# Kernel tuning notes

Measured on AMD Instinct MI355X. Metric: run time of the kernel, lower is better.

## Reference

```python
import jax, jax.numpy as jnp
import numpy as np

H, C = 3, 64  # heads, per-head channels
NEG_SLOPE = 0.2

def setup_inputs() -> dict:
    key = jax.random.key(0)
    ks = jax.random.split(key, 8)
    B, N, D, E = 2, 50000, 128, 800000
    h = jax.random.normal(ks[0], (B, N, D), dtype=jnp.float32)
    edge_index = jax.random.randint(ks[1], (2, E), 0, N, dtype=jnp.int64)
    s = 1.0 / np.sqrt(D)
    W = jax.random.normal(ks[2], (D, H * C), dtype=jnp.float32) * s
    a_src = jax.random.normal(ks[3], (H, C), dtype=jnp.float32) * (1.0 / np.sqrt(C))
    a_dst = jax.random.normal(ks[4], (H, C), dtype=jnp.float32) * (1.0 / np.sqrt(C))
    bias = jnp.zeros((H * C,), dtype=jnp.float32)
    Wo = jax.random.normal(ks[5], (H * C, 1), dtype=jnp.float32) * (1.0 / np.sqrt(H * C))
    bo = jnp.zeros((1,), dtype=jnp.float32)
    return {"h": h, "edge_index": edge_index, "W": W, "a_src": a_src,
            "a_dst": a_dst, "bias": bias, "Wo": Wo, "bo": bo}

def _gat_single(h_b, src, dst, N, W, a_src, a_dst, bias):
    # h_b: [N, D] -> x: [N, H, C]
    x = (h_b @ W).reshape(-1, H, C)
    alpha_s = jnp.einsum('nhc,hc->nh', x, a_src)  # [N, H]
    alpha_d = jnp.einsum('nhc,hc->nh', x, a_dst)  # [N, H]
    e = alpha_s[src] + alpha_d[dst]               # [E', H]
    e = jnp.where(e > 0, e, NEG_SLOPE * e)        # leaky_relu(0.2)
    # segment softmax over edges grouped by destination node
    emax = jax.ops.segment_max(e, dst, num_segments=N)          # [N, H]
    p = jnp.exp(e - emax[dst])
    denom = jax.ops.segment_sum(p, dst, num_segments=N)         # [N, H]
    att = p / (denom[dst] + 1e-16)                               # [E', H]
    out = jax.ops.segment_sum(att[:, :, None] * x[src], dst, num_segments=N)  # [N,H,C]
    return out.reshape(-1, H * C) + bias

def reference(h, edge_index, W, a_src, a_dst, bias, Wo, bo):
    B, N, D = h.shape
    # PyG GATConv default: add self loops
    loops = jnp.arange(N, dtype=edge_index.dtype)
    src = jnp.concatenate([edge_index[0], loops])
    dst = jnp.concatenate([edge_index[1], loops])
    gat = jax.vmap(lambda hb: _gat_single(hb, src, dst, N, W, a_src, a_dst, bias))(h)
    gat = jax.nn.elu(gat)            # [B, N, H*C]; dropout inactive (eval)
    logits = gat @ Wo + bo           # [B, N, 1]
    return logits
```

## Files before the change

### kernel.cpp

```cpp
#include <hip/hip_runtime.h>
#include <hip/hip_bf16.h>
#include <math.h>

typedef __hip_bfloat16 bf16;
typedef __attribute__((ext_vector_type(8))) short short8;
typedef __attribute__((ext_vector_type(4))) float f32x4;

#define HC 192
#define DIN 128
#define NEG_SLOPE 0.2f
#define LCH 64

static inline int cdiv(int a, int b){ return (a + b - 1) / b; }

__device__ inline short f2bf(float f){
  __hip_bfloat16 b = __float2bfloat16(f);
  return __builtin_bit_cast(short, b);
}
__device__ inline float loadf(const void* p, size_t i, int fm){
  return fm ? __bfloat162float(((const bf16*)p)[i]) : ((const float*)p)[i];
}
__device__ inline int eload(const void* p, long long i, int em){
  return em ? (int)(((const long long*)p)[i]) : ((const int*)p)[i];
}

__device__ inline int detect_fm(const unsigned* __restrict__ hw){
  unsigned w = hw[threadIdx.x & 63];
  unsigned expo = (w >> 7) & 0xFF;
  unsigned long long m = __ballot(expo >= 100 && expo <= 135);
  return __popcll(m) > 32;
}
__device__ inline int detect_em(const unsigned* __restrict__ ew){
  unsigned long long m = __ballot(ew[2*(threadIdx.x & 63) + 1] != 0);
  return __popcll(m) < 32;
}

__global__ void k_repack(const void* __restrict__ W, const void* __restrict__ a_src,
    const void* __restrict__ a_dst, const void* __restrict__ bias,
    const void* __restrict__ Wo, const void* __restrict__ bo,
    const unsigned* __restrict__ hw, bf16* __restrict__ Wt,
    float* __restrict__ asf, float* __restrict__ adf, float* __restrict__ biasf,
    float* __restrict__ Wof, float* __restrict__ bof){
  int fm = detect_fm(hw);
  int idx = blockIdx.x * 256 + threadIdx.x;
  if (idx < DIN * HC){
    int d = idx / HC, j = idx - d * HC;
    Wt[j * DIN + d] = __float2bfloat16(loadf(W, idx, fm));
  }
  if (idx < HC){
    asf[idx]   = loadf(a_src, idx, fm);
    adf[idx]   = loadf(a_dst, idx, fm);
    biasf[idx] = loadf(bias, idx, fm);
    Wof[idx]   = loadf(Wo, idx, fm);
  }
  if (idx == 0) bof[0] = loadf(bo, 0, fm);
}

__global__ __launch_bounds__(256) void k_gemm(const void* __restrict__ h,
    const bf16* __restrict__ Wt, bf16* __restrict__ x,
    const float* __restrict__ asf, const float* __restrict__ adf,
    float* __restrict__ asp, float* __restrict__ adp, int M, int N){
  int fm   = detect_fm((const unsigned*)h);
  int tid  = threadIdx.x;
  int w    = tid >> 6;
  int lane = tid & 63;
  int r16  = lane & 15;
  int quad = lane >> 4;
  __shared__ short ldsW[HC * 136];
  for (int c = tid; c < HC * 16; c += 256){
    int row = c >> 4, kg = c & 15;
    *(short8*)&ldsW[row * 136 + kg * 8] = *(const short8*)(Wt + row * DIN + kg * 8);
  }
  __syncthreads();

  int row  = blockIdx.x * 64 + w * 16 + r16;
  int lrow = min(row, M - 1);
  f32x4 acc[12];
  #pragma unroll
  for (int i = 0; i < 12; i++) acc[i] = (f32x4){0.f,0.f,0.f,0.f};
  size_t abase = (size_t)lrow * DIN + quad * 8;
  #pragma unroll
  for (int kb = 0; kb < 4; kb++){
    short8 af;
    if (fm == 0){
      const float* hf = (const float*)h + abase + kb * 32;
      float4 a = *(const float4*)hf;
      float4 b = *(const float4*)(hf + 4);
      af[0]=f2bf(a.x); af[1]=f2bf(a.y); af[2]=f2bf(a.z); af[3]=f2bf(a.w);
      af[4]=f2bf(b.x); af[5]=f2bf(b.y); af[6]=f2bf(b.z); af[7]=f2bf(b.w);
    } else {
      af = *(const short8*)((const bf16*)h + abase + kb * 32);
    }
    #pragma unroll
    for (int nt = 0; nt < 12; nt++){
      short8 bf_ = *(const short8*)&ldsW[(nt*16 + r16) * 136 + kb * 32 + quad * 8];
      acc[nt] = __builtin_amdgcn_mfma_f32_16x16x32_bf16(af, bf_, acc[nt], 0,0,0);
    }
  }
  int rbase = blockIdx.x * 64 + w * 16 + quad * 4;
  #pragma unroll
  for (int nt = 0; nt < 12; nt++){
    #pragma unroll
    for (int r = 0; r < 4; r++){
      int rr = rbase + r;
      if (rr < M) x[(size_t)rr * HC + nt*16 + r16] = __float2bfloat16(acc[nt][r]);
    }
  }
  float asv[12], adv[12];
  #pragma unroll
  for (int nt = 0; nt < 12; nt++){
    int col = (nt >> 2) * 64 + (nt & 3) * 16 + r16;
    asv[nt] = asf[col];
    adv[nt] = adf[col];
  }
  #pragma unroll
  for (int hh = 0; hh < 3; hh++){
    #pragma unroll
    for (int r = 0; r < 4; r++){
      float vs = acc[4*hh+0][r]*asv[4*hh+0] + acc[4*hh+1][r]*asv[4*hh+1]
               + acc[4*hh+2][r]*asv[4*hh+2] + acc[4*hh+3][r]*asv[4*hh+3];
      float vd = acc[4*hh+0][r]*adv[4*hh+0] + acc[4*hh+1][r]*adv[4*hh+1]
               + acc[4*hh+2][r]*adv[4*hh+2] + acc[4*hh+3][r]*adv[4*hh+3];
      #pragma unroll
      for (int off = 8; off; off >>= 1){
        vs += __shfl_down(vs, off, 16);
        vd += __shfl_down(vd, off, 16);
      }
      if (r16 == 0){
        int rr = rbase + r;
        if (rr < M){
          int b = rr >= N;
          int node = rr - b * N;
          asp[(size_t)node*8 + b*3 + hh] = vs;
          adp[(size_t)node*8 + b*3 + hh] = vd;
        }
      }
    }
  }
}

__global__ void k_hist(const void* __restrict__ ei, int E, int N, int* counts){
  int em = detect_em((const unsigned*)ei);
  int idx = blockIdx.x * 256 + threadIdx.x;
  if (idx >= E + N) return;
  int d = (idx < E) ? eload(ei, (long long)E + idx, em) : (idx - E);
  if ((unsigned)d < (unsigned)N) atomicAdd(&counts[d], 1);
}

__global__ __launch_bounds__(256) void k_scanA(const int* __restrict__ counts,
    int* __restrict__ partial, int* __restrict__ bsums, int N){
  __shared__ int s[256];
  int t = threadIdx.x, idx = blockIdx.x * 256 + t;
  int v = (idx < N) ? counts[idx] : 0;
  s[t] = v; __syncthreads();
  for (int o = 1; o < 256; o <<= 1){
    int u = (t >= o) ? s[t - o] : 0;
    __syncthreads();
    s[t] += u;
    __syncthreads();
  }
  if (idx < N) partial[idx] = s[t] - v;
  if (t == 255) bsums[blockIdx.x] = s[255];
}

__global__ __launch_bounds__(256) void k_scanC(const int* __restrict__ partial,
    const int* __restrict__ bsums, int* __restrict__ row_ptr,
    int* __restrict__ cursor, int N, int nb){
  __shared__ int s[256];
  int t = threadIdx.x;
  int v = (t < nb) ? bsums[t] : 0;
  s[t] = v; __syncthreads();
  for (int o = 1; o < 256; o <<= 1){
    int u = (t >= o) ? s[t - o] : 0;
    __syncthreads();
    s[t] += u;
    __syncthreads();
  }
  int excl = s[t] - v;
  __syncthreads();
  s[t] = excl;
  __syncthreads();
  int idx = blockIdx.x * 256 + t;
  int boff = s[blockIdx.x];
  if (idx < N){
    int val = partial[idx] + boff;
    row_ptr[idx] = val;
    cursor[idx]  = val;
  } else if (idx == N){
    row_ptr[N] = s[nb-1] + bsums[nb-1];
  }
}

__global__ void k_scatter(const void* __restrict__ ei, int E, int N,
    int* cursor, const float* __restrict__ asp, const float* __restrict__ adp,
    float* __restrict__ pe){
  int em = detect_em((const unsigned*)ei);
  int idx = blockIdx.x * 256 + threadIdx.x;
  if (idx >= E + N) return;
  int s, d;
  if (idx < E){
    s = eload(ei, idx, em);
    d = eload(ei, (long long)E + idx, em);
  } else { s = d = idx - E; }
  if ((unsigned)d >= (unsigned)N) return;
  if ((unsigned)s >= (unsigned)N) s = 0;
  int p = atomicAdd(&cursor[d], 1);
  const float4* A = (const float4*)asp;
  const float4* D = (const float4*)adp;
  float4 A0 = A[(size_t)s*2], A1 = A[(size_t)s*2 + 1];
  float4 D0 = D[(size_t)d*2], D1 = D[(size_t)d*2 + 1];
  float e0 = A0.x + D0.x, e1 = A0.y + D0.y, e2 = A0.z + D0.z;
  float e3 = A0.w + D0.w, e4 = A1.x + D1.x, e5 = A1.y + D1.y;
  e0 = e0 > 0.f ? e0 : NEG_SLOPE*e0;  e1 = e1 > 0.f ? e1 : NEG_SLOPE*e1;
  e2 = e2 > 0.f ? e2 : NEG_SLOPE*e2;  e3 = e3 > 0.f ? e3 : NEG_SLOPE*e3;
  e4 = e4 > 0.f ? e4 : NEG_SLOPE*e4;  e5 = e5 > 0.f ? e5 : NEG_SLOPE*e5;
  float4 o0 = {__expf(e0), __expf(e1), __expf(e2), __expf(e3)};
  float4 o1 = {__expf(e4), __expf(e5), __int_as_float(s), 0.f};
  float4* pv = (float4*)pe;
  pv[(size_t)p*2]     = o0;
  pv[(size_t)p*2 + 1] = o1;
}

__global__ __launch_bounds__(192) void k_gat(const bf16* __restrict__ x,
    const float* __restrict__ pe, const int* __restrict__ row_ptr,
    const float* __restrict__ biasf, const float* __restrict__ Wof,
    const float* __restrict__ bof, float* __restrict__ out, int N){
  int blk = blockIdx.x;
  int t   = threadIdx.x;
  int nsel = t >= 96;
  int u   = t - nsel * 96;
  int b   = u >= 48;
  int c4  = u - b * 48;
  int hh  = c4 >> 4;
  __shared__ int rp[3];
  __shared__ float ldsP[LCH * 8];
  __shared__ float red[192];
  if (t < 3) rp[t] = row_ptr[2*blk + t];
  __syncthreads();
  int start = rp[nsel], end = rp[nsel + 1];
  int base0 = rp[0], cend = rp[2];
  const ushort* xb = (const ushort*)x + (size_t)b * N * HC + c4 * 4;
  int pidx = b*3 + hh;
  f32x4 acc = {0.f,0.f,0.f,0.f};
  float den = 0.f;
  for (int cb = base0; cb < cend; cb += LCH){
    int cnt = min(LCH, cend - cb);
    __syncthreads();
    if (t < 2*cnt) ((float4*)ldsP)[t] = ((const float4*)pe)[(size_t)cb*2 + t];
    __syncthreads();
    int i0 = max(start, cb), i1 = min(end, cb + cnt);
    #pragma unroll 4
    for (int i = i0; i < i1; i++){
      int rec = i - cb;
      float p = ldsP[rec*8 + pidx];
      int s   = __float_as_int(ldsP[rec*8 + 6]);
      uint2 uu = *(const uint2*)(xb + (size_t)s * HC);
      den += p;
      acc[0] = fmaf(p, __uint_as_float(uu.x << 16),          acc[0]);
      acc[1] = fmaf(p, __uint_as_float(uu.x & 0xffff0000u),  acc[1]);
      acc[2] = fmaf(p, __uint_as_float(uu.y << 16),          acc[2]);
      acc[3] = fmaf(p, __uint_as_float(uu.y & 0xffff0000u),  acc[3]);
    }
  }
  float inv = 1.f / (den + 1e-16f);
  float4 bi = *(const float4*)(biasf + c4*4);
  float4 wo = *(const float4*)(Wof + c4*4);
  float v0 = acc[0]*inv + bi.x;  v0 = v0 > 0.f ? v0 : expm1f(v0);
  float v1 = acc[1]*inv + bi.y;  v1 = v1 > 0.f ? v1 : expm1f(v1);
  float v2 = acc[2]*inv + bi.z;  v2 = v2 > 0.f ? v2 : expm1f(v2);
  float v3 = acc[3]*inv + bi.w;  v3 = v3 > 0.f ? v3 : expm1f(v3);
  red[t] = v0*wo.x + v1*wo.y + v2*wo.z + v3*wo.w;
  __syncthreads();
  if (t < 64){
    int g = t >> 4, l = t & 15;
    float v = red[g*48 + l] + red[g*48 + 16 + l] + red[g*48 + 32 + l];
    v += __shfl_down(v, 8, 16);
    v += __shfl_down(v, 4, 16);
    v += __shfl_down(v, 2, 16);
    v += __shfl_down(v, 1, 16);
    if (l == 0){
      int node = 2*blk + (g >> 1);
      int bb = g & 1;
      out[(size_t)bb * N + node] = v + bof[0];
    }
  }
}

extern "C" void kernel_launch(void* const* d_in, const int* in_sizes, int n_in,
                              void* d_out, int out_size, void* d_ws, size_t ws_size,
                              hipStream_t stream){
  const void* h     = d_in[0];
  const void* ei    = d_in[1];
  const void* W     = d_in[2];
  const void* a_src = d_in[3];
  const void* a_dst = d_in[4];
  const void* bias  = d_in[5];
  const void* Wo    = d_in[6];
  const void* bo    = d_in[7];
  float* out = (float*)d_out;

  const int M    = in_sizes[0] / DIN;
  const int N    = M / 2;
  const int E    = in_sizes[1] / 2;
  const int Etot = E + N;

  char* ws = (char*)d_ws;
  size_t off = 0;
  auto alloc = [&](size_t bytes) -> void* {
    void* p = ws + off;
    off = (off + bytes + 511) & ~(size_t)511;
    return p;
  };
  bf16*  x       = (bf16*) alloc((size_t)M * HC * sizeof(bf16));
  float* asp     = (float*)alloc((size_t)N * 8 * sizeof(float));
  float* adp     = (float*)alloc((size_t)N * 8 * sizeof(float));
  int*   counts  = (int*)  alloc((size_t)N * sizeof(int));
  int*   partial = (int*)  alloc((size_t)N * sizeof(int));
  int*   row_ptr = (int*)  alloc((size_t)(N + 1) * sizeof(int));
  int*   cursor  = (int*)  alloc((size_t)N * sizeof(int));
  int*   bsums   = (int*)  alloc(256 * sizeof(int));
  float* pe      = (float*)alloc((size_t)Etot * 8 * sizeof(float));
  bf16*  Wt      = (bf16*) alloc((size_t)DIN * HC * sizeof(bf16));
  float* asf     = (float*)alloc(HC * sizeof(float));
  float* adf     = (float*)alloc(HC * sizeof(float));
  float* biasf   = (float*)alloc(HC * sizeof(float));
  float* Wof     = (float*)alloc(HC * sizeof(float));
  float* bof     = (float*)alloc(16 * sizeof(float));
  (void)ws_size; (void)n_in; (void)out_size;

  hipMemsetAsync(counts, 0, (size_t)N * sizeof(int), stream);

  k_repack<<<cdiv(DIN * HC, 256), 256, 0, stream>>>(W, a_src, a_dst, bias, Wo, bo,
      (const unsigned*)h, Wt, asf, adf, biasf, Wof, bof);
  k_gemm<<<cdiv(M, 64), 256, 0, stream>>>(h, Wt, x, asf, adf, asp, adp, M, N);
  k_hist<<<cdiv(Etot, 256), 256, 0, stream>>>(ei, E, N, counts);
  int nb = cdiv(N, 256);
  k_scanA<<<nb, 256, 0, stream>>>(counts, partial, bsums, N);
  k_scanC<<<cdiv(N + 1, 256), 256, 0, stream>>>(partial, bsums, row_ptr, cursor, N, nb);
  k_scatter<<<cdiv(Etot, 256), 256, 0, stream>>>(ei, E, N, cursor, asp, adp, pe);
  k_gat<<<N / 2, 192, 0, stream>>>(x, pe, row_ptr, biasf, Wof, bof, out, N);
}
```

Measured before the change: 298.4 us.

## Fuse edge score computation into aggregation kernel and scatter only source indices

The scatter kernel now writes only the source index per sorted edge (4 bytes instead of 32), and the aggregation kernel computes the leaky-ReLU and exp attention scores itself while loading each edge chunk into shared memory. Each block now handles four nodes, and each thread accumulates eight channels with 16-byte loads instead of four. This is meant to cut global write and read traffic for the per-edge score buffer. The trade-off is redundant gathers of the source attention terms inside the aggregation kernel, and fewer blocks for load balancing across uneven node degrees.

```diff
diff --git a/kernel.cpp b/kernel.cpp
--- a/kernel.cpp
+++ b/kernel.cpp
@@ -9,7 +9,8 @@
 #define HC 192
 #define DIN 128
 #define NEG_SLOPE 0.2f
-#define LCH 64
+#define LCH 128
+#define GN 4
 
 static inline int cdiv(int a, int b){ return (a + b - 1) / b; }
 
@@ -192,8 +193,7 @@
 }
 
 __global__ void k_scatter(const void* __restrict__ ei, int E, int N,
-    int* cursor, const float* __restrict__ asp, const float* __restrict__ adp,
-    float* __restrict__ pe){
+    int* cursor, int* __restrict__ esorted){
   int em = detect_em((const unsigned*)ei);
   int idx = blockIdx.x * 256 + threadIdx.x;
   if (idx >= E + N) return;
@@ -205,48 +205,59 @@
   if ((unsigned)d >= (unsigned)N) return;
   if ((unsigned)s >= (unsigned)N) s = 0;
   int p = atomicAdd(&cursor[d], 1);
-  const float4* A = (const float4*)asp;
-  const float4* D = (const float4*)adp;
-  float4 A0 = A[(size_t)s*2], A1 = A[(size_t)s*2 + 1];
-  float4 D0 = D[(size_t)d*2], D1 = D[(size_t)d*2 + 1];
-  float e0 = A0.x + D0.x, e1 = A0.y + D0.y, e2 = A0.z + D0.z;
-  float e3 = A0.w + D0.w, e4 = A1.x + D1.x, e5 = A1.y + D1.y;
-  e0 = e0 > 0.f ? e0 : NEG_SLOPE*e0;  e1 = e1 > 0.f ? e1 : NEG_SLOPE*e1;
-  e2 = e2 > 0.f ? e2 : NEG_SLOPE*e2;  e3 = e3 > 0.f ? e3 : NEG_SLOPE*e3;
-  e4 = e4 > 0.f ? e4 : NEG_SLOPE*e4;  e5 = e5 > 0.f ? e5 : NEG_SLOPE*e5;
-  float4 o0 = {__expf(e0), __expf(e1), __expf(e2), __expf(e3)};
-  float4 o1 = {__expf(e4), __expf(e5), __int_as_float(s), 0.f};
-  float4* pv = (float4*)pe;
-  pv[(size_t)p*2]     = o0;
-  pv[(size_t)p*2 + 1] = o1;
+  esorted[p] = s;
 }
 
 __global__ __launch_bounds__(192) void k_gat(const bf16* __restrict__ x,
-    const float* __restrict__ pe, const int* __restrict__ row_ptr,
+    const int* __restrict__ esorted, const int* __restrict__ row_ptr,
+    const float* __restrict__ asp, const float* __restrict__ adp,
     const float* __restrict__ biasf, const float* __restrict__ Wof,
     const float* __restrict__ bof, float* __restrict__ out, int N){
-  int blk = blockIdx.x;
-  int t   = threadIdx.x;
-  int nsel = t >= 96;
-  int u   = t - nsel * 96;
-  int b   = u >= 48;
-  int c4  = u - b * 48;
-  int hh  = c4 >> 4;
-  __shared__ int rp[3];
+  int blk  = blockIdx.x;
+  int t    = threadIdx.x;
+  int node = t / 48;
+  int u    = t - node * 48;
+  int b    = u >= 24;
+  int c8   = u - b * 24;
+  int hh   = c8 >> 3;
+  __shared__ int   rp[GN + 1];
+  __shared__ float ldsD[GN * 8];
   __shared__ float ldsP[LCH * 8];
   __shared__ float red[192];
-  if (t < 3) rp[t] = row_ptr[2*blk + t];
-  __syncthreads();
-  int start = rp[nsel], end = rp[nsel + 1];
-  int base0 = rp[0], cend = rp[2];
-  const ushort* xb = (const ushort*)x + (size_t)b * N * HC + c4 * 4;
+  if (t < GN + 1) rp[t] = row_ptr[GN*blk + t];
+  if (t >= 8 && t < 8 + GN*2){
+    int i = t - 8;
+    ((float4*)ldsD)[i] = ((const float4*)adp)[(size_t)(GN*blk + (i>>1))*2 + (i&1)];
+  }
+  __syncthreads();
+  int start = rp[node], end = rp[node + 1];
+  int base0 = rp[0], cend = rp[GN];
+  const ushort* xb = (const ushort*)x + (size_t)b * N * HC + c8 * 8;
   int pidx = b*3 + hh;
-  f32x4 acc = {0.f,0.f,0.f,0.f};
+  float acc[8];
+  #pragma unroll
+  for (int k = 0; k < 8; k++) acc[k] = 0.f;
   float den = 0.f;
   for (int cb = base0; cb < cend; cb += LCH){
     int cnt = min(LCH, cend - cb);
     __syncthreads();
-    if (t < 2*cnt) ((float4*)ldsP)[t] = ((const float4*)pe)[(size_t)cb*2 + t];
+    if (t < cnt){
+      int gi = cb + t;
+      int s  = esorted[gi];
+      int dn = (gi >= rp[1]) + (gi >= rp[2]) + (gi >= rp[3]);
+      float4 A0 = ((const float4*)asp)[(size_t)s*2];
+      float4 A1 = ((const float4*)asp)[(size_t)s*2 + 1];
+      const float* D = &ldsD[dn*8];
+      float e0 = A0.x + D[0], e1 = A0.y + D[1], e2 = A0.z + D[2];
+      float e3 = A0.w + D[3], e4 = A1.x + D[4], e5 = A1.y + D[5];
+      e0 = e0 > 0.f ? e0 : NEG_SLOPE*e0;  e1 = e1 > 0.f ? e1 : NEG_SLOPE*e1;
+      e2 = e2 > 0.f ? e2 : NEG_SLOPE*e2;  e3 = e3 > 0.f ? e3 : NEG_SLOPE*e3;
+      e4 = e4 > 0.f ? e4 : NEG_SLOPE*e4;  e5 = e5 > 0.f ? e5 : NEG_SLOPE*e5;
+      float* P = &ldsP[t*8];
+      P[0] = __expf(e0); P[1] = __expf(e1); P[2] = __expf(e2);
+      P[3] = __expf(e3); P[4] = __expf(e4); P[5] = __expf(e5);
+      P[6] = __int_as_float(s);
+    }
     __syncthreads();
     int i0 = max(start, cb), i1 = min(end, cb + cnt);
     #pragma unroll 4
@@ -254,34 +265,45 @@
       int rec = i - cb;
       float p = ldsP[rec*8 + pidx];
       int s   = __float_as_int(ldsP[rec*8 + 6]);
-      uint2 uu = *(const uint2*)(xb + (size_t)s * HC);
+      uint4 q = *(const uint4*)(xb + (size_t)s * HC);
       den += p;
-      acc[0] = fmaf(p, __uint_as_float(uu.x << 16),          acc[0]);
-      acc[1] = fmaf(p, __uint_as_float(uu.x & 0xffff0000u),  acc[1]);
-      acc[2] = fmaf(p, __uint_as_float(uu.y << 16),          acc[2]);
-      acc[3] = fmaf(p, __uint_as_float(uu.y & 0xffff0000u),  acc[3]);
+      acc[0] = fmaf(p, __uint_as_float(q.x << 16),         acc[0]);
+      acc[1] = fmaf(p, __uint_as_float(q.x & 0xffff0000u), acc[1]);
+      acc[2] = fmaf(p, __uint_as_float(q.y << 16),         acc[2]);
+      acc[3] = fmaf(p, __uint_as_float(q.y & 0xffff0000u), acc[3]);
+      acc[4] = fmaf(p, __uint_as_float(q.z << 16),         acc[4]);
+      acc[5] = fmaf(p, __uint_as_float(q.z & 0xffff0000u), acc[5]);
+      acc[6] = fmaf(p, __uint_as_float(q.w << 16),         acc[6]);
+      acc[7] = fmaf(p, __uint_as_float(q.w & 0xffff0000u), acc[7]);
     }
   }
   float inv = 1.f / (den + 1e-16f);
-  float4 bi = *(const float4*)(biasf + c4*4);
-  float4 wo = *(const float4*)(Wof + c4*4);
-  float v0 = acc[0]*inv + bi.x;  v0 = v0 > 0.f ? v0 : expm1f(v0);
-  float v1 = acc[1]*inv + bi.y;  v1 = v1 > 0.f ? v1 : expm1f(v1);
-  float v2 = acc[2]*inv + bi.z;  v2 = v2 > 0.f ? v2 : expm1f(v2);
-  float v3 = acc[3]*inv + bi.w;  v3 = v3 > 0.f ? v3 : expm1f(v3);
-  red[t] = v0*wo.x + v1*wo.y + v2*wo.z + v3*wo.w;
+  float4 bi0 = ((const float4*)biasf)[c8*2], bi1 = ((const float4*)biasf)[c8*2+1];
+  float4 w0  = ((const float4*)Wof)[c8*2],  w1  = ((const float4*)Wof)[c8*2+1];
+  float r = 0.f;
+  {
+    float v;
+    v = acc[0]*inv + bi0.x; v = v > 0.f ? v : expm1f(v); r += v * w0.x;
+    v = acc[1]*inv + bi0.y; v = v > 0.f ? v : expm1f(v); r += v * w0.y;
+    v = acc[2]*inv + bi0.z; v = v > 0.f ? v : expm1f(v); r += v * w0.z;
+    v = acc[3]*inv + bi0.w; v = v > 0.f ? v : expm1f(v); r += v * w0.w;
+    v = acc[4]*inv + bi1.x; v = v > 0.f ? v : expm1f(v); r += v * w1.x;
+    v = acc[5]*inv + bi1.y; v = v > 0.f ? v : expm1f(v); r += v * w1.y;
+    v = acc[6]*inv + bi1.z; v = v > 0.f ? v : expm1f(v); r += v * w1.z;
+    v = acc[7]*inv + bi1.w; v = v > 0.f ? v : expm1f(v); r += v * w1.w;
+  }
+  red[t] = r;
   __syncthreads();
   if (t < 64){
-    int g = t >> 4, l = t & 15;
-    float v = red[g*48 + l] + red[g*48 + 16 + l] + red[g*48 + 32 + l];
-    v += __shfl_down(v, 8, 16);
-    v += __shfl_down(v, 4, 16);
-    v += __shfl_down(v, 2, 16);
-    v += __shfl_down(v, 1, 16);
+    int g = t >> 3, l = t & 7;
+    float v = red[g*24 + l] + red[g*24 + 8 + l] + red[g*24 + 16 + l];
+    v += __shfl_down(v, 4, 8);
+    v += __shfl_down(v, 2, 8);
+    v += __shfl_down(v, 1, 8);
     if (l == 0){
-      int node = 2*blk + (g >> 1);
+      int nd = GN*blk + (g >> 1);
       int bb = g & 1;
-      out[(size_t)bb * N + node] = v + bof[0];
+      out[(size_t)bb * N + nd] = v + bof[0];
     }
   }
 }
@@ -319,7 +341,7 @@
   int*   row_ptr = (int*)  alloc((size_t)(N + 1) * sizeof(int));
   int*   cursor  = (int*)  alloc((size_t)N * sizeof(int));
   int*   bsums   = (int*)  alloc(256 * sizeof(int));
-  float* pe      = (float*)alloc((size_t)Etot * 8 * sizeof(float));
+  int*   esorted = (int*)  alloc((size_t)Etot * sizeof(int));
   bf16*  Wt      = (bf16*) alloc((size_t)DIN * HC * sizeof(bf16));
   float* asf     = (float*)alloc(HC * sizeof(float));
   float* adf     = (float*)alloc(HC * sizeof(float));
@@ -337,6 +359,6 @@
   int nb = cdiv(N, 256);
   k_scanA<<<nb, 256, 0, stream>>>(counts, partial, bsums, N);
   k_scanC<<<cdiv(N + 1, 256), 256, 0, stream>>>(partial, bsums, row_ptr, cursor, N, nb);
-  k_scatter<<<cdiv(Etot, 256), 256, 0, stream>>>(ei, E, N, cursor, asp, adp, pe);
-  k_gat<<<N / 2, 192, 0, stream>>>(x, pe, row_ptr, biasf, Wof, bof, out, N);
-}
+  k_scatter<<<cdiv(Etot, 256), 256, 0, stream>>>(ei, E, N, cursor, esorted);
+  k_gat<<<N / GN, 192, 0, stream>>>(x, esorted, row_ptr, asp, adp, biasf, Wof, bof, out, N);
+}
```

New measurement: 311.5 us. +4.4%, slower.
